# Kernel tuning notes

Measured on AMD Instinct MI355X. Metric: run time of the kernel, lower is better.

The kernel has to match this reference:

```python
import jax, jax.numpy as jnp
import numpy as np

N_NODES = 100000
N_EDGES = 1600000
D_IN = 128
D_HID = 128


def setup_inputs() -> dict:
    key = jax.random.key(0)
    k1, k2, k3, k4 = jax.random.split(key, 4)
    x = jax.random.normal(k1, (N_NODES, D_IN), dtype=jnp.float32)
    edge_index = jax.random.randint(k2, (2, N_EDGES), 0, N_NODES, dtype=jnp.int32)
    # glorot-style init for the two GCNConv linear weights
    s1 = (6.0 / (D_IN + D_HID)) ** 0.5
    s2 = (6.0 / (D_HID + D_HID)) ** 0.5
    W1 = jax.random.uniform(k3, (D_IN, D_HID), dtype=jnp.float32, minval=-s1, maxval=s1)
    W2 = jax.random.uniform(k4, (D_HID, D_HID), dtype=jnp.float32, minval=-s2, maxval=s2)
    b1 = jnp.zeros((D_HID,), dtype=jnp.float32)
    b2 = jnp.zeros((D_HID,), dtype=jnp.float32)
    return {"x": x, "edge_index": edge_index, "W1": W1, "b1": b1, "W2": W2, "b2": b2}


def _gcn_conv(h, src, dst, norm, W, b, num_nodes):
    # PyG GCNConv: linear transform, then normalized scatter-add aggregation, then bias.
    h = h @ W                                   # [N, D]
    msg = h[src] * norm[:, None]                # [E+N, D] gathered + scaled messages
    agg = jax.ops.segment_sum(msg, dst, num_segments=num_nodes)
    return agg + b


def reference(x, edge_index, W1, b1, W2, b2):
    n = x.shape[0]
    loops = jnp.arange(n, dtype=edge_index.dtype)
    src = jnp.concatenate([edge_index[0], loops])  # add self-loops
    dst = jnp.concatenate([edge_index[1], loops])
    # symmetric normalization D^{-1/2} (A+I) D^{-1/2}, degree computed on targets
    deg = jax.ops.segment_sum(jnp.ones_like(dst, dtype=x.dtype), dst, num_segments=n)
    dinv = jnp.where(deg > 0, jax.lax.rsqrt(jnp.maximum(deg, 1.0)), 0.0)
    norm = dinv[src] * dinv[dst]
    h = jax.nn.relu(_gcn_conv(x, src, dst, norm, W1, b1, n))
    h = jax.nn.relu(_gcn_conv(h, src, dst, norm, W2, b2, n))
    return h
```

## Files before the change

### kernel.cpp

```cpp
#include <hip/hip_runtime.h>

#define D 128
#define BSH 8
#define BNODES (1 << BSH)
#define NCHUNK 512
#define MAXB 512

typedef __attribute__((ext_vector_type(8))) __bf16 bf16x8;
typedef __attribute__((ext_vector_type(4))) float f32x4;

__device__ __forceinline__ unsigned short f2bf(float f) {
    unsigned int u = __float_as_uint(f);
    u += 0x7fffu + ((u >> 16) & 1u);
    return (unsigned short)(u >> 16);
}
__device__ __forceinline__ float lo_f(unsigned u) { return __uint_as_float(u << 16); }
__device__ __forceinline__ float hi_f(unsigned u) { return __uint_as_float(u & 0xffff0000u); }


__global__ __launch_bounds__(256) void k_hist(const int* __restrict__ dst,
                                              int* __restrict__ cnts,
                                              int E, int nbkt, int chunk) {
    __shared__ int hist[MAXB];
    int c = blockIdx.x;
    int t = threadIdx.x;
    for (int i = t; i < nbkt; i += 256) hist[i] = 0;
    __syncthreads();
    int e0 = c * chunk, e1 = min(e0 + chunk, E);
    for (int e = e0 + t; e < e1; e += 256) atomicAdd(&hist[dst[e] >> BSH], 1);
    __syncthreads();
    for (int i = t; i < nbkt; i += 256) cnts[(size_t)i * NCHUNK + c] = hist[i];
}

__global__ __launch_bounds__(256) void k_chunksum(int* __restrict__ cnts,
                                                  int* __restrict__ btot, int nbkt) {
    int b = blockIdx.x * 4 + (threadIdx.x >> 6);
    if (b >= nbkt) return;
    int l = threadIdx.x & 63;
    int carry = 0;
    for (int g = 0; g < NCHUNK; g += 64) {
        int v = cnts[(size_t)b * NCHUNK + g + l];
        int x = v;
#pragma unroll
        for (int off = 1; off < 64; off <<= 1) {
            int u = __shfl_up(x, off);
            if (l >= off) x += u;
        }
        cnts[(size_t)b * NCHUNK + g + l] = carry + x - v;
        carry += __shfl(x, 63);
    }
    if (l == 0) btot[b] = carry;
}

__global__ __launch_bounds__(MAXB) void k_bktscan(const int* __restrict__ btot,
                                                  int* __restrict__ bbase, int nbkt) {
    __shared__ int s[MAXB];
    int t = threadIdx.x;
    int v = (t < nbkt) ? btot[t] : 0;
    s[t] = v;
    __syncthreads();
    for (int off = 1; off < MAXB; off <<= 1) {
        int u = (t >= off) ? s[t - off] : 0;
        __syncthreads();
        s[t] += u;
        __syncthreads();
    }
    if (t < nbkt) bbase[t + 1] = s[t];
    if (t == 0) bbase[0] = 0;
}

__global__ __launch_bounds__(256) void k_place(const int* __restrict__ src,
                                               const int* __restrict__ dst,
                                               const int* __restrict__ cnts,
                                               const int* __restrict__ bbase,
                                               unsigned* __restrict__ pairs,
                                               int E, int nbkt, int chunk) {
    __shared__ int cur[MAXB];
    int c = blockIdx.x;
    int t = threadIdx.x;
    for (int i = t; i < nbkt; i += 256)
        cur[i] = bbase[i] + cnts[(size_t)i * NCHUNK + c];
    __syncthreads();
    int e0 = c * chunk, e1 = min(e0 + chunk, E);
    for (int e = e0 + t; e < e1; e += 256) {
        int d = dst[e];
        int p = atomicAdd(&cur[d >> BSH], 1);
        pairs[p] = ((unsigned)(d & (BNODES - 1)) << 24) | (unsigned)src[e];
    }
}

__global__ __launch_bounds__(BNODES) void k_build(const unsigned* __restrict__ pairs,
                                                  const int* __restrict__ bbase,
                                                  int* __restrict__ rp,
                                                  float* __restrict__ dinv,
                                                  int* __restrict__ col, int N) {
    __shared__ int cntL[BNODES];
    __shared__ int lcur[BNODES];
    __shared__ int wsum[BNODES / 64];
    int b = blockIdx.x;
    int n0 = b << BSH;
    int t = threadIdx.x;
    int lane = t & 63, wid = t >> 6;
    int e0 = bbase[b], e1 = bbase[b + 1];

    cntL[t] = 0;
    __syncthreads();
    for (int e = e0 + t; e < e1; e += BNODES)
        atomicAdd(&cntL[pairs[e] >> 24], 1);
    __syncthreads();
    int deg = cntL[t];
    int x = deg;
#pragma unroll
    for (int off = 1; off < 64; off <<= 1) {
        int u = __shfl_up(x, off);
        if (lane >= off) x += u;
    }
    if (lane == 63) wsum[wid] = x;
    __syncthreads();
    int wbase = 0;
#pragma unroll
    for (int i = 0; i < BNODES / 64; ++i) wbase += (i < wid) ? wsum[i] : 0;
    int rpv = e0 + wbase + x - deg;
    lcur[t] = rpv;
    int node = n0 + t;
    if (node < N) {
        rp[node] = rpv;
        dinv[node] = rsqrtf((float)deg + 1.0f);
        if (node == N - 1) rp[N] = e1;
    }
    __syncthreads();
    for (int e = e0 + t; e < e1; e += BNODES) {
        unsigned v = pairs[e];
        int p = atomicAdd(&lcur[v >> 24], 1);
        col[p] = (int)(v & 0x00FFFFFFu);
    }
}

__global__ __launch_bounds__(256) void k_cvt(const float* __restrict__ x,
                                             const float* __restrict__ dinv,
                                             unsigned short* __restrict__ y, int nchunk) {
    int g = blockIdx.x * blockDim.x + threadIdx.x;
    if (g >= nchunk) return;
    int row = g >> 5;
    float s = dinv[row];
    float4 v = reinterpret_cast<const float4*>(x)[g];
    ushort4 o;
    o.x = f2bf(v.x * s);
    o.y = f2bf(v.y * s);
    o.z = f2bf(v.z * s);
    o.w = f2bf(v.w * s);
    reinterpret_cast<ushort4*>(y)[g] = o;
}

__global__ __launch_bounds__(256) void k_wcvt(const float* __restrict__ W1,
                                              const float* __restrict__ W2,
                                              unsigned short* __restrict__ Wt1,
                                              unsigned short* __restrict__ Wt2) {
    int idx = blockIdx.x * 256 + threadIdx.x;
    const float* W = (idx < 16384) ? W1 : W2;
    unsigned short* Wt = (idx < 16384) ? Wt1 : Wt2;
    int i = idx & 16383;
    int c = i >> 7, k = i & 127;
    Wt[(size_t)c * 128 + k] = f2bf(W[(size_t)k * 128 + c]);
}

__global__ __launch_bounds__(128) void k_agg(const unsigned short* __restrict__ y,
                                             unsigned* __restrict__ outp,
                                             const int* __restrict__ col,
                                             const int* __restrict__ rp,
                                             const float* __restrict__ dinv, int n) {
    int node = blockIdx.x * 2 + (threadIdx.x >> 6);
    if (node >= n) return;
    int c = threadIdx.x & 63;
    const unsigned* yv = reinterpret_cast<const unsigned*>(y);

    unsigned v = yv[(size_t)node * 64 + c];
    float a0 = lo_f(v), a1 = hi_f(v);

    int e0 = rp[node], e1 = rp[node + 1];
    int e = e0;
    for (; e + 16 <= e1; e += 16) {
        int s[16];
#pragma unroll
        for (int j = 0; j < 16; ++j) s[j] = col[e + j];
        unsigned u[16];
#pragma unroll
        for (int j = 0; j < 16; ++j) u[j] = yv[(size_t)s[j] * 64 + c];
#pragma unroll
        for (int j = 0; j < 16; ++j) { a0 += lo_f(u[j]); a1 += hi_f(u[j]); }
    }
    for (; e + 8 <= e1; e += 8) {
        int s[8];
#pragma unroll
        for (int j = 0; j < 8; ++j) s[j] = col[e + j];
        unsigned u[8];
#pragma unroll
        for (int j = 0; j < 8; ++j) u[j] = yv[(size_t)s[j] * 64 + c];
#pragma unroll
        for (int j = 0; j < 8; ++j) { a0 += lo_f(u[j]); a1 += hi_f(u[j]); }
    }
    for (; e + 4 <= e1; e += 4) {
        int s0 = col[e], s1 = col[e + 1], s2 = col[e + 2], s3 = col[e + 3];
        unsigned u0 = yv[(size_t)s0 * 64 + c];
        unsigned u1 = yv[(size_t)s1 * 64 + c];
        unsigned u2 = yv[(size_t)s2 * 64 + c];
        unsigned u3 = yv[(size_t)s3 * 64 + c];
        a0 += (lo_f(u0) + lo_f(u1)) + (lo_f(u2) + lo_f(u3));
        a1 += (hi_f(u0) + hi_f(u1)) + (hi_f(u2) + hi_f(u3));
    }
    for (; e < e1; ++e) {
        unsigned u = yv[(size_t)col[e] * 64 + c];
        a0 += lo_f(u);
        a1 += hi_f(u);
    }
    float dn = dinv[node];
    unsigned o = ((unsigned)f2bf(a1 * dn) << 16) | (unsigned)f2bf(a0 * dn);
    outp[(size_t)node * 64 + c] = o;
}

template <int STORE_BF16>
__global__ __launch_bounds__(256) void k_mfma(const unsigned short* __restrict__ A,
                                              const unsigned short* __restrict__ Wt,
                                              const float* __restrict__ bias,
                                              float* __restrict__ out_f32,
                                              unsigned short* __restrict__ out_bf16,
                                              const float* __restrict__ dinv, int N) {
    int tid = threadIdx.x;
    int wv = tid >> 6, l = tid & 63;
    int lr = l & 15, lg = l >> 4;
    int r0 = blockIdx.x * 128 + wv * 32;

    f32x4 acc[2][8];
#pragma unroll
    for (int mi = 0; mi < 2; ++mi)
#pragma unroll
        for (int nf = 0; nf < 8; ++nf) acc[mi][nf] = (f32x4)(0.0f);

#pragma unroll
    for (int k0 = 0; k0 < 128; k0 += 32) {
        bf16x8 a[2];
#pragma unroll
        for (int mi = 0; mi < 2; ++mi) {
            int r = r0 + mi * 16 + lr;
            if (r >= N) r = N - 1;
            a[mi] = *reinterpret_cast<const bf16x8*>(&A[(size_t)r * 128 + k0 + lg * 8]);
        }
#pragma unroll
        for (int nf = 0; nf < 8; ++nf) {
            bf16x8 bw = *reinterpret_cast<const bf16x8*>(
                &Wt[(size_t)(nf * 16 + lr) * 128 + k0 + lg * 8]);
            acc[0][nf] = __builtin_amdgcn_mfma_f32_16x16x32_bf16(bw, a[0], acc[0][nf], 0, 0, 0);
            acc[1][nf] = __builtin_amdgcn_mfma_f32_16x16x32_bf16(bw, a[1], acc[1][nf], 0, 0, 0);
        }
    }

    float4 bv4[8];
#pragma unroll
    for (int nf = 0; nf < 8; ++nf)
        bv4[nf] = *reinterpret_cast<const float4*>(&bias[nf * 16 + lg * 4]);

#pragma unroll
    for (int mi = 0; mi < 2; ++mi) {
        int r = r0 + mi * 16 + lr;
        if (r < N) {
            float dv = 1.0f;
            if (STORE_BF16) dv = dinv[r];
#pragma unroll
            for (int nf = 0; nf < 8; ++nf) {
                float v0 = fmaxf(acc[mi][nf][0] + bv4[nf].x, 0.0f);
                float v1 = fmaxf(acc[mi][nf][1] + bv4[nf].y, 0.0f);
                float v2 = fmaxf(acc[mi][nf][2] + bv4[nf].z, 0.0f);
                float v3 = fmaxf(acc[mi][nf][3] + bv4[nf].w, 0.0f);
                if (STORE_BF16) {
                    uint2 o;
                    o.x = ((unsigned)f2bf(v1 * dv) << 16) | (unsigned)f2bf(v0 * dv);
                    o.y = ((unsigned)f2bf(v3 * dv) << 16) | (unsigned)f2bf(v2 * dv);
                    *reinterpret_cast<uint2*>(&out_bf16[(size_t)r * 128 + nf * 16 + lg * 4]) = o;
                } else {
                    *reinterpret_cast<float4*>(&out_f32[(size_t)r * 128 + nf * 16 + lg * 4]) =
                        make_float4(v0, v1, v2, v3);
                }
            }
        }
    }
}


extern "C" void kernel_launch(void* const* d_in, const int* in_sizes, int n_in,
                              void* d_out, int out_size, void* d_ws, size_t ws_size,
                              hipStream_t stream) {
    const float* x  = (const float*)d_in[0];
    const int*   ei = (const int*)d_in[1];
    const float* W1 = (const float*)d_in[2];
    const float* b1 = (const float*)d_in[3];
    const float* W2 = (const float*)d_in[4];
    const float* b2 = (const float*)d_in[5];
    float* out = (float*)d_out;

    const int N = in_sizes[0] / D;
    const int E = in_sizes[1] / 2;
    const int* src = ei;
    const int* dst = ei + E;
    const int NBKT = (N + BNODES - 1) >> BSH;
    const int CHUNK = (E + NCHUNK - 1) / NCHUNK;

    char* w = (char*)d_ws;
    auto alloc = [&](size_t bytes) -> void* {
        void* p = (void*)w;
        w += (bytes + 255) & ~(size_t)255;
        return p;
    };
    float* dinv     = (float*)alloc((size_t)N * 4);
    int* rp         = (int*)alloc((size_t)(N + 1) * 4);
    int* cnts       = (int*)alloc((size_t)NBKT * NCHUNK * 4);
    int* btot       = (int*)alloc((size_t)NBKT * 4);
    int* bbase      = (int*)alloc((size_t)(NBKT + 1) * 4);
    unsigned* pairs = (unsigned*)alloc((size_t)E * 4);
    int* col        = (int*)alloc((size_t)E * 4);
    unsigned short* y    = (unsigned short*)alloc((size_t)N * D * 2);
    unsigned short* y2   = (unsigned short*)alloc((size_t)N * D * 2);
    unsigned short* Abuf = (unsigned short*)alloc((size_t)N * D * 2);
    unsigned short* Wt1  = (unsigned short*)alloc((size_t)D * D * 2);
    unsigned short* Wt2  = (unsigned short*)alloc((size_t)D * D * 2);

    k_hist<<<NCHUNK, 256, 0, stream>>>(dst, cnts, E, NBKT, CHUNK);
    k_chunksum<<<(NBKT + 3) / 4, 256, 0, stream>>>(cnts, btot, NBKT);
    k_bktscan<<<1, MAXB, 0, stream>>>(btot, bbase, NBKT);
    k_place<<<NCHUNK, 256, 0, stream>>>(src, dst, cnts, bbase, pairs, E, NBKT, CHUNK);
    k_build<<<NBKT, BNODES, 0, stream>>>(pairs, bbase, rp, dinv, col, N);
    k_wcvt<<<128, 256, 0, stream>>>(W1, W2, Wt1, Wt2);

    const int nchunk = N * (D / 4);
    const int aggblocks = (N + 1) / 2;
    const int gemmblocks = (N + 127) / 128;

    k_cvt<<<(nchunk + 255) / 256, 256, 0, stream>>>(x, dinv, y, nchunk);
    k_agg<<<aggblocks, 128, 0, stream>>>(y, (unsigned*)Abuf, col, rp, dinv, N);
    k_mfma<1><<<gemmblocks, 256, 0, stream>>>(Abuf, Wt1, b1, nullptr, y2, dinv, N);
    k_agg<<<aggblocks, 128, 0, stream>>>(y2, (unsigned*)Abuf, col, rp, dinv, N);
    k_mfma<0><<<gemmblocks, 256, 0, stream>>>(Abuf, Wt2, b2, out, nullptr, dinv, N);
}
```

Before: 242.2 us.

## Compute per-node degree in histogram pass and fold weight conversion into it

The histogram kernel now also does a global per-node atomic degree count and carries extra blocks that convert and transpose the weights, replacing the separate weight-conversion launch. The chunk-scan kernel gets extra blocks that compute dinv from the global counts. The build kernel reads the degree directly instead of making its own shared-memory counting pass over the pairs. This removes one kernel launch and one read of the pairs array, at the cost of a memset and 1.6M global atomics on the counts array.

```diff
diff --git a/kernel.cpp b/kernel.cpp
--- a/kernel.cpp
+++ b/kernel.cpp
@@ -18,25 +18,53 @@
 __device__ __forceinline__ float hi_f(unsigned u) { return __uint_as_float(u & 0xffff0000u); }
 
 
-__global__ __launch_bounds__(256) void k_hist(const int* __restrict__ dst,
-                                              int* __restrict__ cnts,
-                                              int E, int nbkt, int chunk) {
+__global__ __launch_bounds__(256) void k_histc(const int* __restrict__ dst,
+                                               int* __restrict__ cnt,
+                                               int* __restrict__ cnts,
+                                               int E, int nbkt, int chunk,
+                                               const float* __restrict__ W1,
+                                               const float* __restrict__ W2,
+                                               unsigned short* __restrict__ Wt1,
+                                               unsigned short* __restrict__ Wt2) {
+    int c = blockIdx.x;
+    int t = threadIdx.x;
+    if (c >= NCHUNK) {
+        int idx = (c - NCHUNK) * 256 + t;
+        const float* W = (idx < 16384) ? W1 : W2;
+        unsigned short* Wt = (idx < 16384) ? Wt1 : Wt2;
+        int i = idx & 16383;
+        int cc = i >> 7, k = i & 127;
+        Wt[(size_t)cc * 128 + k] = f2bf(W[(size_t)k * 128 + cc]);
+        return;
+    }
     __shared__ int hist[MAXB];
-    int c = blockIdx.x;
-    int t = threadIdx.x;
     for (int i = t; i < nbkt; i += 256) hist[i] = 0;
     __syncthreads();
     int e0 = c * chunk, e1 = min(e0 + chunk, E);
-    for (int e = e0 + t; e < e1; e += 256) atomicAdd(&hist[dst[e] >> BSH], 1);
+    for (int e = e0 + t; e < e1; e += 256) {
+        int d = dst[e];
+        atomicAdd(&cnt[d], 1);
+        atomicAdd(&hist[d >> BSH], 1);
+    }
     __syncthreads();
     for (int i = t; i < nbkt; i += 256) cnts[(size_t)i * NCHUNK + c] = hist[i];
 }
 
 __global__ __launch_bounds__(256) void k_chunksum(int* __restrict__ cnts,
-                                                  int* __restrict__ btot, int nbkt) {
-    int b = blockIdx.x * 4 + (threadIdx.x >> 6);
+                                                  int* __restrict__ btot,
+                                                  const int* __restrict__ cnt,
+                                                  float* __restrict__ dinv,
+                                                  int nbkt, int nscan, int N) {
+    int bid = blockIdx.x;
+    int t = threadIdx.x;
+    if (bid >= nscan) {
+        int i = (bid - nscan) * 256 + t;
+        if (i < N) dinv[i] = rsqrtf((float)cnt[i] + 1.0f);
+        return;
+    }
+    int b = bid * 4 + (t >> 6);
     if (b >= nbkt) return;
-    int l = threadIdx.x & 63;
+    int l = t & 63;
     int carry = 0;
     for (int g = 0; g < NCHUNK; g += 64) {
         int v = cnts[(size_t)b * NCHUNK + g + l];
@@ -91,10 +119,9 @@
 
 __global__ __launch_bounds__(BNODES) void k_build(const unsigned* __restrict__ pairs,
                                                   const int* __restrict__ bbase,
+                                                  const int* __restrict__ cnt,
                                                   int* __restrict__ rp,
-                                                  float* __restrict__ dinv,
                                                   int* __restrict__ col, int N) {
-    __shared__ int cntL[BNODES];
     __shared__ int lcur[BNODES];
     __shared__ int wsum[BNODES / 64];
     int b = blockIdx.x;
@@ -102,13 +129,9 @@
     int t = threadIdx.x;
     int lane = t & 63, wid = t >> 6;
     int e0 = bbase[b], e1 = bbase[b + 1];
-
-    cntL[t] = 0;
-    __syncthreads();
-    for (int e = e0 + t; e < e1; e += BNODES)
-        atomicAdd(&cntL[pairs[e] >> 24], 1);
-    __syncthreads();
-    int deg = cntL[t];
+    int node = n0 + t;
+
+    int deg = (node < N) ? cnt[node] : 0;
     int x = deg;
 #pragma unroll
     for (int off = 1; off < 64; off <<= 1) {
@@ -122,10 +145,8 @@
     for (int i = 0; i < BNODES / 64; ++i) wbase += (i < wid) ? wsum[i] : 0;
     int rpv = e0 + wbase + x - deg;
     lcur[t] = rpv;
-    int node = n0 + t;
     if (node < N) {
         rp[node] = rpv;
-        dinv[node] = rsqrtf((float)deg + 1.0f);
         if (node == N - 1) rp[N] = e1;
     }
     __syncthreads();
@@ -150,18 +171,6 @@
     o.z = f2bf(v.z * s);
     o.w = f2bf(v.w * s);
     reinterpret_cast<ushort4*>(y)[g] = o;
-}
-
-__global__ __launch_bounds__(256) void k_wcvt(const float* __restrict__ W1,
-                                              const float* __restrict__ W2,
-                                              unsigned short* __restrict__ Wt1,
-                                              unsigned short* __restrict__ Wt2) {
-    int idx = blockIdx.x * 256 + threadIdx.x;
-    const float* W = (idx < 16384) ? W1 : W2;
-    unsigned short* Wt = (idx < 16384) ? Wt1 : Wt2;
-    int i = idx & 16383;
-    int c = i >> 7, k = i & 127;
-    Wt[(size_t)c * 128 + k] = f2bf(W[(size_t)k * 128 + c]);
 }
 
 __global__ __launch_bounds__(128) void k_agg(const unsigned short* __restrict__ y,
@@ -311,6 +320,7 @@
         return p;
     };
     float* dinv     = (float*)alloc((size_t)N * 4);
+    int* cnt        = (int*)alloc((size_t)N * 4);
     int* rp         = (int*)alloc((size_t)(N + 1) * 4);
     int* cnts       = (int*)alloc((size_t)NBKT * NCHUNK * 4);
     int* btot       = (int*)alloc((size_t)NBKT * 4);
@@ -323,16 +333,20 @@
     unsigned short* Wt1  = (unsigned short*)alloc((size_t)D * D * 2);
     unsigned short* Wt2  = (unsigned short*)alloc((size_t)D * D * 2);
 
-    k_hist<<<NCHUNK, 256, 0, stream>>>(dst, cnts, E, NBKT, CHUNK);
-    k_chunksum<<<(NBKT + 3) / 4, 256, 0, stream>>>(cnts, btot, NBKT);
-    k_bktscan<<<1, MAXB, 0, stream>>>(btot, bbase, NBKT);
-    k_place<<<NCHUNK, 256, 0, stream>>>(src, dst, cnts, bbase, pairs, E, NBKT, CHUNK);
-    k_build<<<NBKT, BNODES, 0, stream>>>(pairs, bbase, rp, dinv, col, N);
-    k_wcvt<<<128, 256, 0, stream>>>(W1, W2, Wt1, Wt2);
-
+    const int nscan = (NBKT + 3) / 4;
+    const int dinvblocks = (N + 255) / 256;
     const int nchunk = N * (D / 4);
     const int aggblocks = (N + 1) / 2;
     const int gemmblocks = (N + 127) / 128;
+
+    hipMemsetAsync(cnt, 0, (size_t)N * 4, stream);
+    k_histc<<<NCHUNK + 128, 256, 0, stream>>>(dst, cnt, cnts, E, NBKT, CHUNK,
+                                              W1, W2, Wt1, Wt2);
+    k_chunksum<<<nscan + dinvblocks, 256, 0, stream>>>(cnts, btot, cnt, dinv,
+                                                       NBKT, nscan, N);
+    k_bktscan<<<1, MAXB, 0, stream>>>(btot, bbase, NBKT);
+    k_place<<<NCHUNK, 256, 0, stream>>>(src, dst, cnts, bbase, pairs, E, NBKT, CHUNK);
+    k_build<<<NBKT, BNODES, 0, stream>>>(pairs, bbase, cnt, rp, col, N);
 
     k_cvt<<<(nchunk + 255) / 256, 256, 0, stream>>>(x, dinv, y, nchunk);
     k_agg<<<aggblocks, 128, 0, stream>>>(y, (unsigned*)Abuf, col, rp, dinv, N);
```

Result: slower. 302.3 us (+24.8%).
